# Optimization experiments

Measured on AMD Instinct MI355X. Metric: run time of the kernel, lower is better.

Reference implementation:

```python
import jax, jax.numpy as jnp
import numpy as np

B, H, SQ, SK, D = 2, 16, 2048, 2048, 128
INV_SCALE = 0.05  # scores are DIVIDED by this (i.e., multiplied by 20)


def setup_inputs() -> dict:
    k0 = jax.random.key(0)
    kq, kk, kv, km = jax.random.split(k0, 4)
    query = jax.random.normal(kq, (B, H, SQ, D), dtype=jnp.float32)
    key = jax.random.normal(kk, (B, H, SK, D), dtype=jnp.float32)
    value = jax.random.normal(kv, (B, H, SK, D), dtype=jnp.float32)
    padding_mask = jax.random.randint(km, (D,), 0, 2).astype(jnp.bool_)
    input_mask = jnp.zeros((D,), dtype=jnp.bool_)  # unused by forward, kept for signature parity
    return {"query": query, "key": key, "value": value,
            "padding_mask": padding_mask, "input_mask": input_mask}


def reference(query, key, value, padding_mask, input_mask):
    # scores: [B, H, SQ, SK]
    qk = jnp.einsum('bhqd,bhkd->bhqk', query, key)
    attn = jax.nn.softmax(qk / INV_SCALE, axis=-1)
    # dropout with undefined dropout_p in source; eval mode -> identity
    out = jnp.einsum('bhqk,bhkd->bhqd', attn, value)  # [B, H, SQ, D]
    # masked_fill over the LAST (head) dim, per padding_mask[None,None,None,:]
    out = jnp.where(padding_mask[None, None, None, :], jnp.float32(0.0), out)
    return out
```

## Files before the change

kernel.cpp:

```cpp
#include <hip/hip_runtime.h>
#include <math.h>

#define SQ_ 2048
#define SK_ 2048
#define D_  128
#define BH_ 32
#define SCALE 20.0f

typedef __attribute__((ext_vector_type(8))) __bf16 bf16x8;
typedef __attribute__((ext_vector_type(4))) __bf16 bf16x4;
typedef __attribute__((ext_vector_type(2))) __bf16 bf16x2;
typedef __attribute__((ext_vector_type(4))) float  floatx4;

#define PSTR 40
#define TILE_ELEMS 12288
#define WS_NEED ((size_t)BH_ * 64 * TILE_ELEMS * 2)

typedef __attribute__((address_space(3))) unsigned int lds_uint;
typedef const __attribute__((address_space(1))) unsigned int glob_uint;
__device__ __forceinline__ void async16(const void* g, void* l) {
    __builtin_amdgcn_global_load_lds((glob_uint*)g, (lds_uint*)l, 16, 0, 0);
}

template<int CTRL>
__device__ __forceinline__ float dpp_maxstep(float x) {
    int xi = __builtin_bit_cast(int, x);
    int yi = __builtin_amdgcn_update_dpp(xi, xi, CTRL, 0xF, 0xF, false);
    return fmaxf(x, __builtin_bit_cast(float, yi));
}
__device__ __forceinline__ float rowmax16(float x) {
    x = dpp_maxstep<0xB1>(x);
    x = dpp_maxstep<0x4E>(x);
    x = dpp_maxstep<0x141>(x);
    x = dpp_maxstep<0x140>(x);
    return x;
}

__global__ void prep_k2(const float* __restrict__ K, __bf16* __restrict__ ws)
{
    const int kt = blockIdx.x & 63, bh = blockIdx.x >> 6;
    const int t = threadIdx.x;
    const float* src = K + ((size_t)(bh * SK_ + kt * 32)) * D_;
    __bf16* tile = ws + (size_t)(bh * 64 + kt) * TILE_ELEMS;
#pragma unroll
    for (int h = 0; h < 2; ++h) {
        const int tt = t + h * 256;
        const int key = tt >> 4, c4q = tt & 15;
        floatx4 a = *(const floatx4*)(src + tt * 8);
        floatx4 b = *(const floatx4*)(src + tt * 8 + 4);
        bf16x8 hi, lo;
#pragma unroll
        for (int j = 0; j < 4; ++j) {
            __bf16 x = (__bf16)a[j]; hi[j] = x; lo[j] = (__bf16)(a[j] - (float)x);
        }
#pragma unroll
        for (int j = 0; j < 4; ++j) {
            __bf16 x = (__bf16)b[j]; hi[4 + j] = x; lo[4 + j] = (__bf16)(b[j] - (float)x);
        }
        const int g = c4q * 32 + key;
        *(bf16x8*)(tile + g * 8) = hi;
        *(bf16x8*)(tile + 4096 + g * 8) = lo;
    }
}

__global__ void prep_v2(const float* __restrict__ V, __bf16* __restrict__ ws)
{
    const int kt = blockIdx.x & 63, bh = blockIdx.x >> 6;
    const int t = threadIdx.x;
    const float* src = V + ((size_t)(bh * SK_ + kt * 32)) * D_;
    __bf16* tile = ws + (size_t)(bh * 64 + kt) * TILE_ELEMS + 8192;
#pragma unroll
    for (int h = 0; h < 2; ++h) {
        const int g = t + h * 256;
        const int d = g & 127, quad = g >> 7;
        bf16x8 p;
#pragma unroll
        for (int e = 0; e < 8; ++e)
            p[e] = (__bf16)src[(quad * 8 + e) * D_ + d];
        *(bf16x8*)(tile + g * 8) = p;
    }
}

__global__ __launch_bounds__(256, 2)
void fattn3(const float* __restrict__ Q, const __bf16* __restrict__ ws,
            const int* __restrict__ mask, float* __restrict__ Out)
{
    __shared__ __align__(16) __bf16 sTile[2][TILE_ELEMS];
    __shared__ __align__(16) __bf16 sP[4 * 32 * PSTR];

    const int tid  = threadIdx.x;
    const int w    = tid >> 6;
    const int lane = tid & 63;
    const int m    = lane & 15;
    const int quad = lane >> 4;
    const int id = blockIdx.x;
    const int bh = (id & 7) * 4 + ((id >> 3) & 3);
    const int qt = id >> 5;

    bf16x8 qhi[2][4], qlo[2][4];
#pragma unroll
    for (int rt = 0; rt < 2; ++rt) {
        const int qrow = qt * 128 + w * 32 + rt * 16 + m;
        const float* qp = Q + ((size_t)(bh * SQ_ + qrow)) * D_;
#pragma unroll
        for (int c = 0; c < 4; ++c) {
            const int d0 = c * 32 + quad * 8;
            floatx4 a = *(const floatx4*)(qp + d0);
            floatx4 b = *(const floatx4*)(qp + d0 + 4);
#pragma unroll
            for (int j = 0; j < 4; ++j) {
                float x = a[j] * SCALE;
                __bf16 h = (__bf16)x;
                qhi[rt][c][j] = h; qlo[rt][c][j] = (__bf16)(x - (float)h);
            }
#pragma unroll
            for (int j = 0; j < 4; ++j) {
                float x = b[j] * SCALE;
                __bf16 h = (__bf16)x;
                qhi[rt][c][4 + j] = h; qlo[rt][c][4 + j] = (__bf16)(x - (float)h);
            }
        }
    }

    bf16x8 vones;
#pragma unroll
    for (int j = 0; j < 8; ++j) vones[j] = (__bf16)1.0f;

    floatx4 O[2][8], lac[2];
#pragma unroll
    for (int rt = 0; rt < 2; ++rt) {
        lac[rt] = (floatx4){0.f, 0.f, 0.f, 0.f};
#pragma unroll
        for (int t = 0; t < 8; ++t) O[rt][t] = (floatx4){0.f, 0.f, 0.f, 0.f};
    }
    float m_i[2][4];
#pragma unroll
    for (int rt = 0; rt < 2; ++rt)
#pragma unroll
        for (int r = 0; r < 4; ++r) m_i[rt][r] = -INFINITY;

    const __bf16* wsB = ws + (size_t)bh * 64 * TILE_ELEMS;
    __bf16* sPw = sP + w * 32 * PSTR;

#pragma unroll
    for (int j6 = 0; j6 < 6; ++j6) {
        const int j = w * 6 + j6;
        async16(wsB + j * 512 + lane * 8, &sTile[0][j * 512]);
    }

    for (int kt = 0; kt < SK_ / 32; ++kt) {
        const int buf = kt & 1;
        __syncthreads();

        if (kt < SK_ / 32 - 1) {
            const __bf16* wsT = wsB + (size_t)(kt + 1) * TILE_ELEMS;
#pragma unroll
            for (int j6 = 0; j6 < 6; ++j6) {
                const int j = w * 6 + j6;
                async16(wsT + j * 512 + lane * 8, &sTile[buf ^ 1][j * 512]);
            }
        }

        const __bf16* khi = &sTile[buf][0];
        const __bf16* klo = khi + 4096;
        const __bf16* vt  = khi + 8192;

        floatx4 S[2][2];
#pragma unroll
        for (int rt = 0; rt < 2; ++rt)
#pragma unroll
            for (int nt = 0; nt < 2; ++nt) S[rt][nt] = (floatx4){0.f, 0.f, 0.f, 0.f};
#pragma unroll
        for (int nt = 0; nt < 2; ++nt) {
#pragma unroll
            for (int c = 0; c < 4; ++c) {
                const int off = (((c * 4 + quad) * 32) + nt * 16 + m) * 8;
                bf16x8 kh = *(const bf16x8*)(khi + off);
                bf16x8 kl = *(const bf16x8*)(klo + off);
#pragma unroll
                for (int rt = 0; rt < 2; ++rt) {
                    S[rt][nt] = __builtin_amdgcn_mfma_f32_16x16x32_bf16(qhi[rt][c], kh, S[rt][nt], 0, 0, 0);
                    S[rt][nt] = __builtin_amdgcn_mfma_f32_16x16x32_bf16(qlo[rt][c], kh, S[rt][nt], 0, 0, 0);
                    S[rt][nt] = __builtin_amdgcn_mfma_f32_16x16x32_bf16(qhi[rt][c], kl, S[rt][nt], 0, 0, 0);
                }
            }
        }

#pragma unroll
        for (int rt = 0; rt < 2; ++rt) {
            float alpha[4];
#pragma unroll
            for (int r = 0; r < 4; ++r) {
                const float tmax = rowmax16(fmaxf(S[rt][0][r], S[rt][1][r]));
                const float mn = fmaxf(m_i[rt][r], tmax);
                alpha[r] = __expf(m_i[rt][r] - mn);
                S[rt][0][r] = __expf(S[rt][0][r] - mn);
                S[rt][1][r] = __expf(S[rt][1][r] - mn);
                m_i[rt][r] = mn;
            }
#pragma unroll
            for (int r = 0; r < 4; ++r) lac[rt][r] *= alpha[r];
#pragma unroll
            for (int t = 0; t < 8; ++t)
#pragma unroll
                for (int r = 0; r < 4; ++r)
                    O[rt][t][r] *= alpha[r];
        }

#pragma unroll
        for (int rt = 0; rt < 2; ++rt)
#pragma unroll
            for (int r = 0; r < 4; ++r) {
                sPw[(rt * 16 + quad * 4 + r) * PSTR + m]      = (__bf16)S[rt][0][r];
                sPw[(rt * 16 + quad * 4 + r) * PSTR + 16 + m] = (__bf16)S[rt][1][r];
            }
        __asm__ volatile("s_waitcnt lgkmcnt(0)" ::: "memory");
        bf16x8 pf0 = *(const bf16x8*)&sPw[m * PSTR + quad * 8];
        bf16x8 pf1 = *(const bf16x8*)&sPw[(16 + m) * PSTR + quad * 8];

        lac[0] = __builtin_amdgcn_mfma_f32_16x16x32_bf16(pf0, vones, lac[0], 0, 0, 0);
        lac[1] = __builtin_amdgcn_mfma_f32_16x16x32_bf16(pf1, vones, lac[1], 0, 0, 0);
#pragma unroll
        for (int t = 0; t < 8; ++t) {
            bf16x8 vf = *(const bf16x8*)(vt + (quad * 128 + t * 16 + m) * 8);
            O[0][t] = __builtin_amdgcn_mfma_f32_16x16x32_bf16(pf0, vf, O[0][t], 0, 0, 0);
            O[1][t] = __builtin_amdgcn_mfma_f32_16x16x32_bf16(pf1, vf, O[1][t], 0, 0, 0);
        }
    }

#pragma unroll
    for (int rt = 0; rt < 2; ++rt) {
        float inv[4];
#pragma unroll
        for (int r = 0; r < 4; ++r) inv[r] = 1.0f / lac[rt][r];
        const int qrow0 = qt * 128 + w * 32 + rt * 16 + quad * 4;
        float* outp = Out + ((size_t)(bh * SQ_ + qrow0)) * D_;
#pragma unroll
        for (int t = 0; t < 8; ++t) {
            const int d = t * 16 + m;
            const float mk = (mask[d] != 0) ? 0.0f : 1.0f;
#pragma unroll
            for (int r = 0; r < 4; ++r)
                outp[r * D_ + d] = O[rt][t][r] * inv[r] * mk;
        }
    }
}

#define KSTR 136
#define VSTR 40
__global__ __launch_bounds__(256, 2)
void fattn_kernel(const float* __restrict__ Q, const float* __restrict__ K,
                  const float* __restrict__ V, const int* __restrict__ mask,
                  float* __restrict__ Out)
{
    __shared__ __align__(16) __bf16 sKhi[32 * KSTR];
    __shared__ __align__(16) __bf16 sKlo[32 * KSTR];
    __shared__ __align__(16) __bf16 sVt[128 * VSTR];
    __shared__ __align__(16) __bf16 sP2[4 * 16 * PSTR];

    const int tid  = threadIdx.x;
    const int w    = tid >> 6;
    const int lane = tid & 63;
    const int m    = lane & 15;
    const int quad = lane >> 4;
    const int qt   = blockIdx.x;
    const int bh   = blockIdx.y;

    bf16x8 qhi[4], qlo[4];
    {
        const int qrow = qt * 64 + w * 16 + m;
        const float* qp = Q + ((size_t)(bh * SQ_ + qrow)) * D_;
#pragma unroll
        for (int c = 0; c < 4; ++c) {
            const int d0 = c * 32 + quad * 8;
            floatx4 a = *(const floatx4*)(qp + d0);
            floatx4 b = *(const floatx4*)(qp + d0 + 4);
#pragma unroll
            for (int j = 0; j < 4; ++j) {
                float x = a[j] * SCALE;
                __bf16 h = (__bf16)x;
                qhi[c][j] = h; qlo[c][j] = (__bf16)(x - (float)h);
            }
#pragma unroll
            for (int j = 0; j < 4; ++j) {
                float x = b[j] * SCALE;
                __bf16 h = (__bf16)x;
                qhi[c][4 + j] = h; qlo[c][4 + j] = (__bf16)(x - (float)h);
            }
        }
    }

    floatx4 O[8];
#pragma unroll
    for (int t = 0; t < 8; ++t) O[t] = (floatx4){0.f, 0.f, 0.f, 0.f};
    float m_i[4] = {-INFINITY, -INFINITY, -INFINITY, -INFINITY};
    float l_i[4] = {0.f, 0.f, 0.f, 0.f};

    const float* Kbh = K + (size_t)bh * SK_ * D_;
    const float* Vbh = V + (size_t)bh * SK_ * D_;
    __bf16* sPw = sP2 + w * 16 * PSTR;

    for (int kt = 0; kt < SK_ / 32; ++kt) {
        const int kbase = kt * 32;
#pragma unroll
        for (int i = 0; i < 4; ++i) {
            const int lin = i * 1024 + tid * 4;
            const int key = lin >> 7;
            const int d   = lin & 127;
            floatx4 v = *(const floatx4*)(Kbh + (kbase + key) * D_ + d);
            bf16x4 h4, l4;
#pragma unroll
            for (int j = 0; j < 4; ++j) {
                __bf16 h = (__bf16)v[j]; h4[j] = h; l4[j] = (__bf16)(v[j] - (float)h);
            }
            *(bf16x4*)&sKhi[key * KSTR + d] = h4;
            *(bf16x4*)&sKlo[key * KSTR + d] = l4;
        }
#pragma unroll
        for (int i = 0; i < 2; ++i) {
            const int pi   = i * 256 + tid;
            const int kp   = (pi & 15) * 2;
            const int dblk = (pi >> 4);
            const int d0   = dblk * 4;
            floatx4 v0 = *(const floatx4*)(Vbh + (kbase + kp) * D_ + d0);
            floatx4 v1 = *(const floatx4*)(Vbh + (kbase + kp + 1) * D_ + d0);
#pragma unroll
            for (int j = 0; j < 4; ++j) {
                bf16x2 p2; p2[0] = (__bf16)v0[j]; p2[1] = (__bf16)v1[j];
                *(bf16x2*)&sVt[(d0 + j) * VSTR + kp] = p2;
            }
        }
        __syncthreads();

        floatx4 Sv[2];
#pragma unroll
        for (int nt = 0; nt < 2; ++nt) {
            floatx4 acc = (floatx4){0.f, 0.f, 0.f, 0.f};
#pragma unroll
            for (int c = 0; c < 4; ++c) {
                const int off = (nt * 16 + m) * KSTR + c * 32 + quad * 8;
                bf16x8 kh = *(const bf16x8*)&sKhi[off];
                bf16x8 kl = *(const bf16x8*)&sKlo[off];
                acc = __builtin_amdgcn_mfma_f32_16x16x32_bf16(qhi[c], kh, acc, 0, 0, 0);
                acc = __builtin_amdgcn_mfma_f32_16x16x32_bf16(qlo[c], kh, acc, 0, 0, 0);
                acc = __builtin_amdgcn_mfma_f32_16x16x32_bf16(qhi[c], kl, acc, 0, 0, 0);
            }
            Sv[nt] = acc;
        }

        float alpha[4];
#pragma unroll
        for (int r = 0; r < 4; ++r) {
            float tmax = fmaxf(Sv[0][r], Sv[1][r]);
#pragma unroll
            for (int off = 1; off < 16; off <<= 1)
                tmax = fmaxf(tmax, __shfl_xor(tmax, off, 64));
            const float mn = fmaxf(m_i[r], tmax);
            const float a  = __expf(m_i[r] - mn);
            const float p0 = __expf(Sv[0][r] - mn);
            const float p1 = __expf(Sv[1][r] - mn);
            Sv[0][r] = p0; Sv[1][r] = p1;
            float rs = p0 + p1;
#pragma unroll
            for (int off = 1; off < 16; off <<= 1)
                rs += __shfl_xor(rs, off, 64);
            l_i[r] = l_i[r] * a + rs;
            m_i[r] = mn;
            alpha[r] = a;
        }
#pragma unroll
        for (int t = 0; t < 8; ++t)
#pragma unroll
            for (int r = 0; r < 4; ++r)
                O[t][r] *= alpha[r];

#pragma unroll
        for (int r = 0; r < 4; ++r) {
            sPw[(quad * 4 + r) * PSTR + m]      = (__bf16)Sv[0][r];
            sPw[(quad * 4 + r) * PSTR + 16 + m] = (__bf16)Sv[1][r];
        }
        __asm__ volatile("s_waitcnt lgkmcnt(0)" ::: "memory");
        bf16x8 pf = *(const bf16x8*)&sPw[m * PSTR + quad * 8];

#pragma unroll
        for (int t = 0; t < 8; ++t) {
            bf16x8 vf = *(const bf16x8*)&sVt[(t * 16 + m) * VSTR + quad * 8];
            O[t] = __builtin_amdgcn_mfma_f32_16x16x32_bf16(pf, vf, O[t], 0, 0, 0);
        }
        __syncthreads();
    }

    float inv[4];
#pragma unroll
    for (int r = 0; r < 4; ++r) inv[r] = 1.0f / l_i[r];
    const int qrow0 = qt * 64 + w * 16 + quad * 4;
    float* outp = Out + ((size_t)(bh * SQ_ + qrow0)) * D_;
#pragma unroll
    for (int t = 0; t < 8; ++t) {
        const int d = t * 16 + m;
        const float mk = (mask[d] != 0) ? 0.0f : 1.0f;
#pragma unroll
        for (int r = 0; r < 4; ++r)
            outp[r * D_ + d] = O[t][r] * inv[r] * mk;
    }
}

extern "C" void kernel_launch(void* const* d_in, const int* in_sizes, int n_in,
                              void* d_out, int out_size, void* d_ws, size_t ws_size,
                              hipStream_t stream) {
    const float* Q = (const float*)d_in[0];
    const float* K = (const float*)d_in[1];
    const float* V = (const float*)d_in[2];
    const int* mask = (const int*)d_in[3];
    float* out = (float*)d_out;

    if (ws_size >= WS_NEED) {
        __bf16* ws = (__bf16*)d_ws;
        prep_k2<<<2048, 256, 0, stream>>>(K, ws);
        prep_v2<<<2048, 256, 0, stream>>>(V, ws);
        fattn3<<<512, 256, 0, stream>>>(Q, ws, mask, out);
    } else {
        dim3 grid(SQ_ / 64, BH_);
        fattn_kernel<<<grid, 256, 0, stream>>>(Q, K, V, mask, out);
    }
}
```

Before: 300.8 us.

## Rewrite attention path with fp16 split-precision, lazy rescaling, and 64-key tiles

Replaces the bf16 hi/lo pipeline with fp16 hi/lo splitting, folds log2(e) into the query scale so exp2 replaces exp, and processes 64-key tiles in a single LDS buffer. K and V prefetch are staggered around two barriers. The P matrix stays in registers by computing S transposed, which removes the per-tile LDS round trip. The running max is only rescaled when it grows past a threshold, skipping most alpha multiplies. The two prep kernels are fused into one that transposes through shared memory. Risks include fp16 overflow or precision loss in the unrescaled exponentials and less overlap from the single-buffered tile.

```diff
diff --git a/kernel.cpp b/kernel.cpp
--- a/kernel.cpp
+++ b/kernel.cpp
@@ -5,16 +5,19 @@
 #define SK_ 2048
 #define D_  128
 #define BH_ 32
-#define SCALE 20.0f
-
+#define SCALE_L2E 28.853900817779268f
+#define TAU 13.0f
+
+typedef _Float16 f16;
+typedef __attribute__((ext_vector_type(8))) f16    f16x8;
+typedef __attribute__((ext_vector_type(4))) f16    f16x4;
+typedef __attribute__((ext_vector_type(4))) float  floatx4;
 typedef __attribute__((ext_vector_type(8))) __bf16 bf16x8;
 typedef __attribute__((ext_vector_type(4))) __bf16 bf16x4;
 typedef __attribute__((ext_vector_type(2))) __bf16 bf16x2;
-typedef __attribute__((ext_vector_type(4))) float  floatx4;
-
-#define PSTR 40
-#define TILE_ELEMS 12288
-#define WS_NEED ((size_t)BH_ * 64 * TILE_ELEMS * 2)
+
+#define TILE_ELEMS 24576
+#define WS_NEED ((size_t)BH_ * 32 * TILE_ELEMS * 2)
 
 typedef __attribute__((address_space(3))) unsigned int lds_uint;
 typedef const __attribute__((address_space(1))) unsigned int glob_uint;
@@ -22,232 +25,233 @@
     __builtin_amdgcn_global_load_lds((glob_uint*)g, (lds_uint*)l, 16, 0, 0);
 }
 
-template<int CTRL>
-__device__ __forceinline__ float dpp_maxstep(float x) {
-    int xi = __builtin_bit_cast(int, x);
-    int yi = __builtin_amdgcn_update_dpp(xi, xi, CTRL, 0xF, 0xF, false);
-    return fmaxf(x, __builtin_bit_cast(float, yi));
+__global__ void prep(const float* __restrict__ K, const float* __restrict__ V,
+                     f16* __restrict__ ws)
+{
+    __shared__ float sB[64 * 132];
+    const int id = blockIdx.x;
+    const int t  = threadIdx.x;
+    const size_t src_off = ((size_t)(id >> 5) * SK_ + (id & 31) * 64) * D_;
+    f16* tile = ws + (size_t)id * TILE_ELEMS;
+
+    const float* srcK = K + src_off;
+#pragma unroll
+    for (int i = 0; i < 8; ++i) {
+        const int idx = t + i * 256, row = idx >> 5, c4 = (idx & 31) * 4;
+        *(floatx4*)&sB[row * 132 + c4] = *(const floatx4*)(srcK + row * 128 + c4);
+    }
+    __syncthreads();
+#pragma unroll
+    for (int h = 0; h < 4; ++h) {
+        const int g = t + h * 256, key = g & 63, c4q = g >> 6;
+        floatx4 a = *(const floatx4*)&sB[key * 132 + c4q * 8];
+        floatx4 b = *(const floatx4*)&sB[key * 132 + c4q * 8 + 4];
+        f16x8 hi, lo;
+#pragma unroll
+        for (int j = 0; j < 4; ++j) {
+            f16 x = (f16)a[j]; hi[j] = x; lo[j] = (f16)(a[j] - (float)x);
+        }
+#pragma unroll
+        for (int j = 0; j < 4; ++j) {
+            f16 x = (f16)b[j]; hi[4 + j] = x; lo[4 + j] = (f16)(b[j] - (float)x);
+        }
+        *(f16x8*)(tile + g * 8) = hi;
+        *(f16x8*)(tile + 8192 + g * 8) = lo;
+    }
+    __syncthreads();
+    const float* srcV = V + src_off;
+#pragma unroll
+    for (int i = 0; i < 8; ++i) {
+        const int idx = t + i * 256, row = idx >> 5, c4 = (idx & 31) * 4;
+        *(floatx4*)&sB[row * 132 + c4] = *(const floatx4*)(srcV + row * 128 + c4);
+    }
+    __syncthreads();
+#pragma unroll
+    for (int h = 0; h < 4; ++h) {
+        const int g = t + h * 256, kq = g >> 7, d = g & 127;
+        f16x8 p;
+#pragma unroll
+        for (int e = 0; e < 8; ++e) p[e] = (f16)sB[(kq * 8 + e) * 132 + d];
+        *(f16x8*)(tile + 16384 + g * 8) = p;
+    }
 }
-__device__ __forceinline__ float rowmax16(float x) {
-    x = dpp_maxstep<0xB1>(x);
-    x = dpp_maxstep<0x4E>(x);
-    x = dpp_maxstep<0x141>(x);
-    x = dpp_maxstep<0x140>(x);
-    return x;
-}
-
-__global__ void prep_k2(const float* __restrict__ K, __bf16* __restrict__ ws)
-{
-    const int kt = blockIdx.x & 63, bh = blockIdx.x >> 6;
-    const int t = threadIdx.x;
-    const float* src = K + ((size_t)(bh * SK_ + kt * 32)) * D_;
-    __bf16* tile = ws + (size_t)(bh * 64 + kt) * TILE_ELEMS;
-#pragma unroll
-    for (int h = 0; h < 2; ++h) {
-        const int tt = t + h * 256;
-        const int key = tt >> 4, c4q = tt & 15;
-        floatx4 a = *(const floatx4*)(src + tt * 8);
-        floatx4 b = *(const floatx4*)(src + tt * 8 + 4);
-        bf16x8 hi, lo;
-#pragma unroll
-        for (int j = 0; j < 4; ++j) {
-            __bf16 x = (__bf16)a[j]; hi[j] = x; lo[j] = (__bf16)(a[j] - (float)x);
-        }
-#pragma unroll
-        for (int j = 0; j < 4; ++j) {
-            __bf16 x = (__bf16)b[j]; hi[4 + j] = x; lo[4 + j] = (__bf16)(b[j] - (float)x);
-        }
-        const int g = c4q * 32 + key;
-        *(bf16x8*)(tile + g * 8) = hi;
-        *(bf16x8*)(tile + 4096 + g * 8) = lo;
-    }
-}
-
-__global__ void prep_v2(const float* __restrict__ V, __bf16* __restrict__ ws)
-{
-    const int kt = blockIdx.x & 63, bh = blockIdx.x >> 6;
-    const int t = threadIdx.x;
-    const float* src = V + ((size_t)(bh * SK_ + kt * 32)) * D_;
-    __bf16* tile = ws + (size_t)(bh * 64 + kt) * TILE_ELEMS + 8192;
-#pragma unroll
-    for (int h = 0; h < 2; ++h) {
-        const int g = t + h * 256;
-        const int d = g & 127, quad = g >> 7;
-        bf16x8 p;
-#pragma unroll
-        for (int e = 0; e < 8; ++e)
-            p[e] = (__bf16)src[(quad * 8 + e) * D_ + d];
-        *(bf16x8*)(tile + g * 8) = p;
-    }
-}
 
 __global__ __launch_bounds__(256, 2)
-void fattn3(const float* __restrict__ Q, const __bf16* __restrict__ ws,
+void fattn4(const float* __restrict__ Q, const f16* __restrict__ ws,
             const int* __restrict__ mask, float* __restrict__ Out)
 {
-    __shared__ __align__(16) __bf16 sTile[2][TILE_ELEMS];
-    __shared__ __align__(16) __bf16 sP[4 * 32 * PSTR];
+    __shared__ __align__(16) f16 sT[TILE_ELEMS];
 
     const int tid  = threadIdx.x;
     const int w    = tid >> 6;
     const int lane = tid & 63;
     const int m    = lane & 15;
     const int quad = lane >> 4;
-    const int id = blockIdx.x;
-    const int bh = (id & 7) * 4 + ((id >> 3) & 3);
-    const int qt = id >> 5;
-
-    bf16x8 qhi[2][4], qlo[2][4];
+    const int id   = blockIdx.x;
+    const int bh   = (id & 7) * 4 + ((id >> 3) & 3);
+    const int qt   = id >> 5;
+
+    f16x8 qhi[2][4], qlo[2][4];
 #pragma unroll
     for (int rt = 0; rt < 2; ++rt) {
         const int qrow = qt * 128 + w * 32 + rt * 16 + m;
         const float* qp = Q + ((size_t)(bh * SQ_ + qrow)) * D_;
 #pragma unroll
         for (int c = 0; c < 4; ++c) {
-            const int d0 = c * 32 + quad * 8;
-            floatx4 a = *(const floatx4*)(qp + d0);
-            floatx4 b = *(const floatx4*)(qp + d0 + 4);
-#pragma unroll
-            for (int j = 0; j < 4; ++j) {
-                float x = a[j] * SCALE;
-                __bf16 h = (__bf16)x;
-                qhi[rt][c][j] = h; qlo[rt][c][j] = (__bf16)(x - (float)h);
-            }
-#pragma unroll
-            for (int j = 0; j < 4; ++j) {
-                float x = b[j] * SCALE;
-                __bf16 h = (__bf16)x;
-                qhi[rt][c][4 + j] = h; qlo[rt][c][4 + j] = (__bf16)(x - (float)h);
-            }
-        }
-    }
-
-    bf16x8 vones;
-#pragma unroll
-    for (int j = 0; j < 8; ++j) vones[j] = (__bf16)1.0f;
+            floatx4 a = *(const floatx4*)(qp + c * 32 + quad * 8);
+            floatx4 b = *(const floatx4*)(qp + c * 32 + quad * 8 + 4);
+#pragma unroll
+            for (int j = 0; j < 4; ++j) {
+                float x = a[j] * SCALE_L2E;
+                f16 h = (f16)x;
+                qhi[rt][c][j] = h; qlo[rt][c][j] = (f16)(x - (float)h);
+            }
+#pragma unroll
+            for (int j = 0; j < 4; ++j) {
+                float x = b[j] * SCALE_L2E;
+                f16 h = (f16)x;
+                qhi[rt][c][4 + j] = h; qlo[rt][c][4 + j] = (f16)(x - (float)h);
+            }
+        }
+    }
+
+    f16x4 ones4;
+#pragma unroll
+    for (int j = 0; j < 4; ++j) ones4[j] = (f16)1.0f;
 
     floatx4 O[2][8], lac[2];
+    float mf[2] = {-INFINITY, -INFINITY};
 #pragma unroll
     for (int rt = 0; rt < 2; ++rt) {
         lac[rt] = (floatx4){0.f, 0.f, 0.f, 0.f};
 #pragma unroll
         for (int t = 0; t < 8; ++t) O[rt][t] = (floatx4){0.f, 0.f, 0.f, 0.f};
     }
-    float m_i[2][4];
-#pragma unroll
-    for (int rt = 0; rt < 2; ++rt)
-#pragma unroll
-        for (int r = 0; r < 4; ++r) m_i[rt][r] = -INFINITY;
-
-    const __bf16* wsB = ws + (size_t)bh * 64 * TILE_ELEMS;
-    __bf16* sPw = sP + w * 32 * PSTR;
-
-#pragma unroll
-    for (int j6 = 0; j6 < 6; ++j6) {
-        const int j = w * 6 + j6;
-        async16(wsB + j * 512 + lane * 8, &sTile[0][j * 512]);
-    }
-
-    for (int kt = 0; kt < SK_ / 32; ++kt) {
-        const int buf = kt & 1;
+
+    const f16* wsB = ws + (size_t)bh * 32 * TILE_ELEMS;
+
+#pragma unroll
+    for (int j = 0; j < 8; ++j)
+        async16(wsB + (w * 8 + j) * 512 + lane * 8, &sT[(w * 8 + j) * 512]);
+#pragma unroll
+    for (int j = 0; j < 4; ++j)
+        async16(wsB + 16384 + (w * 4 + j) * 512 + lane * 8, &sT[16384 + (w * 4 + j) * 512]);
+    __syncthreads();
+
+    for (int kt = 0; kt < 32; ++kt) {
+        floatx4 S[2][4];
+#pragma unroll
+        for (int rt = 0; rt < 2; ++rt)
+#pragma unroll
+            for (int nt = 0; nt < 4; ++nt) S[rt][nt] = (floatx4){0.f, 0.f, 0.f, 0.f};
+#pragma unroll
+        for (int c = 0; c < 4; ++c) {
+#pragma unroll
+            for (int nt = 0; nt < 4; ++nt) {
+                const int g = (c * 4 + quad) * 64 + nt * 16 + m;
+                f16x8 kh = *(const f16x8*)&sT[g * 8];
+                f16x8 kl = *(const f16x8*)&sT[8192 + g * 8];
+#pragma unroll
+                for (int rt = 0; rt < 2; ++rt) {
+                    S[rt][nt] = __builtin_amdgcn_mfma_f32_16x16x32_f16(kh, qhi[rt][c], S[rt][nt], 0, 0, 0);
+                    S[rt][nt] = __builtin_amdgcn_mfma_f32_16x16x32_f16(kl, qhi[rt][c], S[rt][nt], 0, 0, 0);
+                    S[rt][nt] = __builtin_amdgcn_mfma_f32_16x16x32_f16(kh, qlo[rt][c], S[rt][nt], 0, 0, 0);
+                }
+            }
+        }
+
         __syncthreads();
-
-        if (kt < SK_ / 32 - 1) {
-            const __bf16* wsT = wsB + (size_t)(kt + 1) * TILE_ELEMS;
-#pragma unroll
-            for (int j6 = 0; j6 < 6; ++j6) {
-                const int j = w * 6 + j6;
-                async16(wsT + j * 512 + lane * 8, &sTile[buf ^ 1][j * 512]);
-            }
-        }
-
-        const __bf16* khi = &sTile[buf][0];
-        const __bf16* klo = khi + 4096;
-        const __bf16* vt  = khi + 8192;
-
-        floatx4 S[2][2];
+        if (kt + 1 < 32) {
+            const f16* nk = wsB + (size_t)(kt + 1) * TILE_ELEMS;
+#pragma unroll
+            for (int j = 0; j < 8; ++j)
+                async16(nk + (w * 8 + j) * 512 + lane * 8, &sT[(w * 8 + j) * 512]);
+        }
+
+        float mx[2];
+#pragma unroll
+        for (int rt = 0; rt < 2; ++rt) {
+            float v0 = fmaxf(fmaxf(S[rt][0][0], S[rt][0][1]), fmaxf(S[rt][0][2], S[rt][0][3]));
+            float v1 = fmaxf(fmaxf(S[rt][1][0], S[rt][1][1]), fmaxf(S[rt][1][2], S[rt][1][3]));
+            float v2 = fmaxf(fmaxf(S[rt][2][0], S[rt][2][1]), fmaxf(S[rt][2][2], S[rt][2][3]));
+            float v3 = fmaxf(fmaxf(S[rt][3][0], S[rt][3][1]), fmaxf(S[rt][3][2], S[rt][3][3]));
+            float v = fmaxf(fmaxf(v0, v1), fmaxf(v2, v3));
+            v = fmaxf(v, __shfl_xor(v, 16));
+            v = fmaxf(v, __shfl_xor(v, 32));
+            mx[rt] = v;
+        }
+        const bool upd = (mx[0] > mf[0] + TAU) || (mx[1] > mf[1] + TAU);
+        if (__ballot(upd)) {
+#pragma unroll
+            for (int rt = 0; rt < 2; ++rt) {
+                const float mn = fmaxf(mf[rt], mx[rt]);
+                const float al = exp2f(mf[rt] - mn);
+                mf[rt] = mn;
+                lac[rt][0] *= al;
+#pragma unroll
+                for (int t = 0; t < 8; ++t)
+#pragma unroll
+                    for (int r = 0; r < 4; ++r) O[rt][t][r] *= al;
+            }
+        }
+
+        f16x4 P[2][4];
 #pragma unroll
         for (int rt = 0; rt < 2; ++rt)
 #pragma unroll
-            for (int nt = 0; nt < 2; ++nt) S[rt][nt] = (floatx4){0.f, 0.f, 0.f, 0.f};
-#pragma unroll
-        for (int nt = 0; nt < 2; ++nt) {
-#pragma unroll
-            for (int c = 0; c < 4; ++c) {
-                const int off = (((c * 4 + quad) * 32) + nt * 16 + m) * 8;
-                bf16x8 kh = *(const bf16x8*)(khi + off);
-                bf16x8 kl = *(const bf16x8*)(klo + off);
-#pragma unroll
-                for (int rt = 0; rt < 2; ++rt) {
-                    S[rt][nt] = __builtin_amdgcn_mfma_f32_16x16x32_bf16(qhi[rt][c], kh, S[rt][nt], 0, 0, 0);
-                    S[rt][nt] = __builtin_amdgcn_mfma_f32_16x16x32_bf16(qlo[rt][c], kh, S[rt][nt], 0, 0, 0);
-                    S[rt][nt] = __builtin_amdgcn_mfma_f32_16x16x32_bf16(qhi[rt][c], kl, S[rt][nt], 0, 0, 0);
-                }
-            }
-        }
-
-#pragma unroll
-        for (int rt = 0; rt < 2; ++rt) {
-            float alpha[4];
+            for (int nt = 0; nt < 4; ++nt)
+#pragma unroll
+                for (int r = 0; r < 4; ++r)
+                    P[rt][nt][r] = (f16)exp2f(S[rt][nt][r] - mf[rt]);
+
+#pragma unroll
+        for (int rt = 0; rt < 2; ++rt)
+#pragma unroll
+            for (int nt = 0; nt < 4; ++nt)
+                lac[rt] = __builtin_amdgcn_mfma_f32_16x16x16f16(ones4, P[rt][nt], lac[rt], 0, 0, 0);
+
+#pragma unroll
+        for (int t = 0; t < 8; ++t) {
+#pragma unroll
+            for (int nt = 0; nt < 4; ++nt) {
+                f16x4 vf = *(const f16x4*)&sT[16384 +
+                    ((nt * 2 + (quad >> 1)) * 128 + t * 16 + m) * 8 + (quad & 1) * 4];
+                O[0][t] = __builtin_amdgcn_mfma_f32_16x16x16f16(vf, P[0][nt], O[0][t], 0, 0, 0);
+                O[1][t] = __builtin_amdgcn_mfma_f32_16x16x16f16(vf, P[1][nt], O[1][t], 0, 0, 0);
+            }
+        }
+
+        __syncthreads();
+        if (kt + 1 < 32) {
+            const f16* nv = wsB + (size_t)(kt + 1) * TILE_ELEMS + 16384;
+#pragma unroll
+            for (int j = 0; j < 4; ++j)
+                async16(nv + (w * 4 + j) * 512 + lane * 8, &sT[16384 + (w * 4 + j) * 512]);
+        }
+    }
+
+#pragma unroll
+    for (int rt = 0; rt < 2; ++rt) {
+        const float inv = 1.0f / lac[rt][0];
+        const int qrow = qt * 128 + w * 32 + rt * 16 + m;
+        float* outp = Out + ((size_t)(bh * SQ_ + qrow)) * D_;
+#pragma unroll
+        for (int t = 0; t < 8; ++t) {
+            const int d0 = t * 16 + quad * 4;
+            floatx4 o;
 #pragma unroll
             for (int r = 0; r < 4; ++r) {
-                const float tmax = rowmax16(fmaxf(S[rt][0][r], S[rt][1][r]));
-                const float mn = fmaxf(m_i[rt][r], tmax);
-                alpha[r] = __expf(m_i[rt][r] - mn);
-                S[rt][0][r] = __expf(S[rt][0][r] - mn);
-                S[rt][1][r] = __expf(S[rt][1][r] - mn);
-                m_i[rt][r] = mn;
-            }
-#pragma unroll
-            for (int r = 0; r < 4; ++r) lac[rt][r] *= alpha[r];
-#pragma unroll
-            for (int t = 0; t < 8; ++t)
-#pragma unroll
-                for (int r = 0; r < 4; ++r)
-                    O[rt][t][r] *= alpha[r];
-        }
-
-#pragma unroll
-        for (int rt = 0; rt < 2; ++rt)
-#pragma unroll
-            for (int r = 0; r < 4; ++r) {
-                sPw[(rt * 16 + quad * 4 + r) * PSTR + m]      = (__bf16)S[rt][0][r];
-                sPw[(rt * 16 + quad * 4 + r) * PSTR + 16 + m] = (__bf16)S[rt][1][r];
-            }
-        __asm__ volatile("s_waitcnt lgkmcnt(0)" ::: "memory");
-        bf16x8 pf0 = *(const bf16x8*)&sPw[m * PSTR + quad * 8];
-        bf16x8 pf1 = *(const bf16x8*)&sPw[(16 + m) * PSTR + quad * 8];
-
-        lac[0] = __builtin_amdgcn_mfma_f32_16x16x32_bf16(pf0, vones, lac[0], 0, 0, 0);
-        lac[1] = __builtin_amdgcn_mfma_f32_16x16x32_bf16(pf1, vones, lac[1], 0, 0, 0);
-#pragma unroll
-        for (int t = 0; t < 8; ++t) {
-            bf16x8 vf = *(const bf16x8*)(vt + (quad * 128 + t * 16 + m) * 8);
-            O[0][t] = __builtin_amdgcn_mfma_f32_16x16x32_bf16(pf0, vf, O[0][t], 0, 0, 0);
-            O[1][t] = __builtin_amdgcn_mfma_f32_16x16x32_bf16(pf1, vf, O[1][t], 0, 0, 0);
-        }
-    }
-
-#pragma unroll
-    for (int rt = 0; rt < 2; ++rt) {
-        float inv[4];
-#pragma unroll
-        for (int r = 0; r < 4; ++r) inv[r] = 1.0f / lac[rt][r];
-        const int qrow0 = qt * 128 + w * 32 + rt * 16 + quad * 4;
-        float* outp = Out + ((size_t)(bh * SQ_ + qrow0)) * D_;
-#pragma unroll
-        for (int t = 0; t < 8; ++t) {
-            const int d = t * 16 + m;
-            const float mk = (mask[d] != 0) ? 0.0f : 1.0f;
-#pragma unroll
-            for (int r = 0; r < 4; ++r)
-                outp[r * D_ + d] = O[rt][t][r] * inv[r] * mk;
+                const float mk = (mask[d0 + r] != 0) ? 0.0f : 1.0f;
+                o[r] = O[rt][t][r] * inv * mk;
+            }
+            *(floatx4*)(outp + d0) = o;
         }
     }
 }
 
 #define KSTR 136
 #define VSTR 40
+#define PSTR 40
 __global__ __launch_bounds__(256, 2)
 void fattn_kernel(const float* __restrict__ Q, const float* __restrict__ K,
                   const float* __restrict__ V, const int* __restrict__ mask,
@@ -277,13 +281,13 @@
             floatx4 b = *(const floatx4*)(qp + d0 + 4);
 #pragma unroll
             for (int j = 0; j < 4; ++j) {
-                float x = a[j] * SCALE;
+                float x = a[j] * 20.0f;
                 __bf16 h = (__bf16)x;
                 qhi[c][j] = h; qlo[c][j] = (__bf16)(x - (float)h);
             }
 #pragma unroll
             for (int j = 0; j < 4; ++j) {
-                float x = b[j] * SCALE;
+                float x = b[j] * 20.0f;
                 __bf16 h = (__bf16)x;
                 qhi[c][4 + j] = h; qlo[c][4 + j] = (__bf16)(x - (float)h);
             }
@@ -415,10 +419,9 @@
     float* out = (float*)d_out;
 
     if (ws_size >= WS_NEED) {
-        __bf16* ws = (__bf16*)d_ws;
-        prep_k2<<<2048, 256, 0, stream>>>(K, ws);
-        prep_v2<<<2048, 256, 0, stream>>>(V, ws);
-        fattn3<<<512, 256, 0, stream>>>(Q, ws, mask, out);
+        f16* ws = (f16*)d_ws;
+        prep<<<1024, 256, 0, stream>>>(K, V, ws);
+        fattn4<<<512, 256, 0, stream>>>(Q, ws, mask, out);
     } else {
         dim3 grid(SQ_ / 64, BH_);
         fattn_kernel<<<grid, 256, 0, stream>>>(Q, K, V, mask, out);
```

After: 276.0 us. -8.2%, faster.
